# Kernel optimization log

Hardware: AMD Instinct MI355X
Metric: run time of the kernel (lower is better)

The kernel has to match this reference:

```python
import jax, jax.numpy as jnp
import numpy as np
import math

VOCAB, D, H, NL, L, B = 50257, 768, 12, 4, 1024, 2
DH = D // H
DFF = 4 * D
ALPHA = 0.25
NEG = -1e9


def _ln(x, g, b, eps=1e-5):
    mu = x.mean(-1, keepdims=True)
    var = ((x - mu) ** 2).mean(-1, keepdims=True)
    return (x - mu) * jax.lax.rsqrt(var + eps) * g + b


def setup_inputs() -> dict:
    key = jax.random.key(0)
    ks = jax.random.split(key, 16)
    s = 0.02
    tokens = jax.random.randint(ks[0], (B, L), 0, VOCAB)
    timelike_mask = jax.random.randint(ks[1], (NL, D), 0, 2).astype(jnp.int32)
    embed = jax.random.normal(ks[2], (VOCAB, D), jnp.float32) * s
    pos_emb = jax.random.normal(ks[3], (L, D), jnp.float32) * s
    wq = jax.random.normal(ks[4], (NL, D, D), jnp.float32) * s
    wk = jax.random.normal(ks[5], (NL, D, D), jnp.float32) * s
    wv = jax.random.normal(ks[6], (NL, D, D), jnp.float32) * s
    wo = jax.random.normal(ks[7], (NL, D, D), jnp.float32) * s
    ff_w1 = jax.random.normal(ks[8], (NL, DFF, D), jnp.float32) * s
    ff_b1 = jnp.zeros((NL, DFF), jnp.float32)
    ff_w2 = jax.random.normal(ks[9], (NL, D, DFF), jnp.float32) * s
    ff_b2 = jnp.zeros((NL, D), jnp.float32)
    ln1_g = jnp.ones((NL, D), jnp.float32); ln1_b = jnp.zeros((NL, D), jnp.float32)
    ln2_g = jnp.ones((NL, D), jnp.float32); ln2_b = jnp.zeros((NL, D), jnp.float32)
    lnf_g = jnp.ones((D,), jnp.float32); lnf_b = jnp.zeros((D,), jnp.float32)
    return dict(tokens=tokens, timelike_mask=timelike_mask, embed=embed, pos_emb=pos_emb,
                wq=wq, wk=wk, wv=wv, wo=wo,
                ln1_g=ln1_g, ln1_b=ln1_b, ln2_g=ln2_g, ln2_b=ln2_b,
                ff_w1=ff_w1, ff_b1=ff_b1, ff_w2=ff_w2, ff_b2=ff_b2,
                lnf_g=lnf_g, lnf_b=lnf_b)


def reference(tokens, timelike_mask, embed, pos_emb, wq, wk, wv, wo,
              ln1_g, ln1_b, ln2_g, ln2_b, ff_w1, ff_b1, ff_w2, ff_b2,
              lnf_g, lnf_b):
    Bc, Lc = tokens.shape
    scale = math.sqrt(DH)
    # embeddings: token + learned position
    h = embed[tokens] + pos_emb[None, :Lc]  # (B,L,D)
    # additive causal mask, matching torch's -inf attention_mask convention
    causal = jnp.where(jnp.tril(jnp.ones((Lc, Lc), bool)), 0.0, NEG)[None, None]  # (1,1,L,L)
    for i in range(NL):
        xn = _ln(h, ln1_g[i], ln1_b[i])
        # nn.Linear(bias=False): y = x @ W.T, W is (out,in)
        q = jnp.einsum('bld,od->blo', xn, wq[i]).reshape(Bc, Lc, H, DH).astype(jnp.float32)
        k = jnp.einsum('bld,od->blo', xn, wk[i]).reshape(Bc, Lc, H, DH).astype(jnp.float32)
        v = jnp.einsum('bld,od->blo', xn, wv[i]).reshape(Bc, Lc, H, DH)
        # Minkowski term: scores_std - 2*alpha*(Q*P_t)K^T  ==  (Q*(1-2*alpha*m)) K^T
        m = timelike_mask[i].astype(jnp.float32).reshape(H, DH)  # per-head timelike directions
        q_eff = q * (1.0 - 2.0 * ALPHA * m)[None, None]
        scores = jnp.einsum('bqhd,bkhd->bhqk', q_eff, k) / scale + causal
        aw = jax.nn.softmax(scores, axis=-1)  # dropout=0 (eval)
        attn = jnp.einsum('bhqk,bkhd->bqhd', aw, v).reshape(Bc, Lc, D)
        h = h + jnp.einsum('bld,od->blo', attn, wo[i])
        xn2 = _ln(h, ln2_g[i], ln2_b[i])
        ff = jax.nn.gelu(jnp.einsum('bld,fd->blf', xn2, ff_w1[i]) + ff_b1[i], approximate=False)
        h = h + jnp.einsum('blf,df->bld', ff, ff_w2[i]) + ff_b2[i]
    h = _ln(h, lnf_g, lnf_b)
    logits = jnp.einsum('bld,vd->blv', h, embed)  # tied LM head
    return logits
```

## Files before the change

### kernel.cpp

```cpp
#include <hip/hip_runtime.h>
#include <math.h>

#define VOCABSZ 50257
#define VPAD 50432
#define DMODEL 768
#define NHEAD 12
#define NLAYER 4
#define SEQ 1024
#define BATCH 2
#define DHEAD 64
#define DFFN 3072
#define BT (BATCH * SEQ)
#define NBH (BATCH * NHEAD)

typedef __attribute__((ext_vector_type(8))) short bf16x8;
typedef __attribute__((ext_vector_type(4))) float f32x4;

__device__ __forceinline__ ushort f2bf(float f) {
  uint u = __builtin_bit_cast(uint, f);
  u = (u + 0x7fffu + ((u >> 16) & 1u)) >> 16;
  return (ushort)u;
}

__device__ __forceinline__ float bf2f(ushort u) {
  uint x = ((uint)u) << 16;
  return __builtin_bit_cast(float, x);
}

__device__ __forceinline__ void gl_lds16(const ushort* g, ushort* l) {
  __builtin_amdgcn_global_load_lds(
      (const __attribute__((address_space(1))) void*)g,
      (__attribute__((address_space(3))) void*)l, 16, 0, 0);
}

__global__ __launch_bounds__(256) void conv4_kernel(
    const float* __restrict__ src, ushort* __restrict__ dst, int n4) {
  int i = blockIdx.x * 256 + threadIdx.x;
  if (i >= n4) return;
  float4 v = reinterpret_cast<const float4*>(src)[i];
  reinterpret_cast<ushort4*>(dst)[i] =
      make_ushort4(f2bf(v.x), f2bf(v.y), f2bf(v.z), f2bf(v.w));
}

__global__ __launch_bounds__(256) void conv_qkv_kernel(
    const float* __restrict__ src, ushort* __restrict__ dst, int qoff4) {
  const int per4 = DMODEL * DMODEL / 4;
  int i = blockIdx.x * 256 + threadIdx.x;
  if (i >= NLAYER * per4) return;
  int layer = i / per4, rem = i % per4;
  float4 v = reinterpret_cast<const float4*>(src)[i];
  reinterpret_cast<ushort4*>(dst)[(size_t)layer * (3 * per4) + qoff4 + rem] =
      make_ushort4(f2bf(v.x), f2bf(v.y), f2bf(v.z), f2bf(v.w));
}

__global__ __launch_bounds__(256) void conv_embed_kernel(
    const float* __restrict__ emb, ushort* __restrict__ dst) {
  int i = blockIdx.x * 256 + threadIdx.x;
  if (i >= VPAD * DMODEL / 4) return;
  int row = (i * 4) / DMODEL;
  ushort4 o = make_ushort4(0, 0, 0, 0);
  if (row < VOCABSZ) {
    float4 v = reinterpret_cast<const float4*>(emb)[i];
    o = make_ushort4(f2bf(v.x), f2bf(v.y), f2bf(v.z), f2bf(v.w));
  }
  reinterpret_cast<ushort4*>(dst)[i] = o;
}

template <int KS, bool RBIAS, bool EMB>
__global__ __launch_bounds__(256) void ln_kernel(
    float* __restrict__ h, const ushort* __restrict__ part,
    const float* __restrict__ rb, const int* __restrict__ tok,
    const float* __restrict__ emb, const float* __restrict__ pos,
    const float* __restrict__ g, const float* __restrict__ bta,
    ushort* __restrict__ o) {
  __shared__ float red[8];
  int row = blockIdx.x;
  int tid = threadIdx.x;
  float* xr = h + (size_t)row * DMODEL;
  const float* er = nullptr;
  const float* pr = nullptr;
  if (EMB) {
    er = emb + (size_t)tok[row] * DMODEL;
    pr = pos + (size_t)(row & (SEQ - 1)) * DMODEL;
  }
  float v[3];
  float s = 0.f, sq = 0.f;
#pragma unroll
  for (int j = 0; j < 3; ++j) {
    int c = tid + j * 256;
    float a;
    if (EMB) {
      a = er[c] + pr[c];
      xr[c] = a;
    } else {
      a = xr[c];
      if (RBIAS) a += rb[c];
      if (KS > 0) {
#pragma unroll
        for (int z = 0; z < KS; ++z)
          a += bf2f(part[(size_t)z * BT * DMODEL + (size_t)row * DMODEL + c]);
        xr[c] = a;
      }
    }
    v[j] = a;
    s += a;
    sq += a * a;
  }
#pragma unroll
  for (int off = 1; off < 64; off <<= 1) {
    s += __shfl_xor(s, off);
    sq += __shfl_xor(sq, off);
  }
  int wid = tid >> 6;
  if ((tid & 63) == 0) { red[wid * 2] = s; red[wid * 2 + 1] = sq; }
  __syncthreads();
  float S = red[0] + red[2] + red[4] + red[6];
  float SQ = red[1] + red[3] + red[5] + red[7];
  float mu = S * (1.0f / DMODEL);
  float var = SQ * (1.0f / DMODEL) - mu * mu;
  float r = rsqrtf(var + 1e-5f);
  ushort* orow = o + (size_t)row * DMODEL;
#pragma unroll
  for (int j = 0; j < 3; ++j) {
    int c = tid + j * 256;
    orow[c] = f2bf((v[j] - mu) * r * g[c] + bta[c]);
  }
}

__global__ __launch_bounds__(256) void fattn_kernel(
    const ushort* __restrict__ q, const ushort* __restrict__ k,
    const ushort* __restrict__ vt, ushort* __restrict__ o) {
  __shared__ __align__(16) ushort Ks[2][64 * 64];
  __shared__ __align__(16) ushort Vs[2][64 * 64];
  __shared__ __align__(16) ushort Ps[4][16][80];
  const int bid = blockIdx.x;
  const int wgid = (bid & 7) * 48 + (bid >> 3);
  const int z = wgid / 16, qb_ = wgid % 16;
  const int b = z / NHEAD, hh = z % NHEAD;
  const int q0 = (15 - qb_) * 64;
  const int tid = threadIdx.x, w = tid >> 6, l = tid & 63;
  const int fr = l & 15, ks = l >> 4;
  const int qrow = q0 + w * 16 + fr;
  const ushort* qp = q + (size_t)(b * SEQ + qrow) * DMODEL + hh * DHEAD;
  const bf16x8 qf0 = *reinterpret_cast<const bf16x8*>(qp + ks * 8);
  const bf16x8 qf1 = *reinterpret_cast<const bf16x8*>(qp + 32 + ks * 8);

  const int srow = w * 16 + (l >> 3);
  const int g0 = ((l & 7) ^ (srow & 7)) * 8;

  auto stage = [&](int k0, int d) {
#pragma unroll
    for (int c = 0; c < 2; ++c) {
      int r = srow + c * 8;
      gl_lds16(k + (size_t)(b * SEQ + k0 + r) * DMODEL + hh * DHEAD + g0,
               &Ks[d][(w * 16 + c * 8) * 64]);
      gl_lds16(vt + (size_t)(z * 64 + r) * SEQ + k0 + g0,
               &Vs[d][(w * 16 + c * 8) * 64]);
    }
  };

  f32x4 acc_o[4] = {};
  float mrun = -1e30f, lrun = 0.f;
  const int nt = q0 >> 6;

  stage(0, 0);
  for (int t = 0; t <= nt; ++t) {
    const int cur = t & 1;
    if (t < nt) {
      stage((t + 1) * 64, cur ^ 1);
      asm volatile("s_waitcnt vmcnt(4)" ::: "memory");
    } else {
      asm volatile("s_waitcnt vmcnt(0)" ::: "memory");
    }
    __builtin_amdgcn_s_barrier();
    __builtin_amdgcn_sched_barrier(0);
    f32x4 acc_s[4] = {};
#pragma unroll
    for (int kstep = 0; kstep < 2; ++kstep) {
      const bf16x8 qf = kstep ? qf1 : qf0;
#pragma unroll
      for (int kb = 0; kb < 4; ++kb) {
        int ra = kb * 16 + fr;
        bf16x8 af = *reinterpret_cast<const bf16x8*>(
            &Ks[cur][ra * 64 + (((kstep * 4 + ks) ^ (ra & 7)) * 8)]);
        acc_s[kb] =
            __builtin_amdgcn_mfma_f32_16x16x32_bf16(af, qf, acc_s[kb], 0, 0, 0);
      }
    }
    const bool diag = (t == nt);
    float pm = -1e30f;
    float sv[4][4];
#pragma unroll
    for (int kb = 0; kb < 4; ++kb)
#pragma unroll
      for (int r = 0; r < 4; ++r) {
        float s = acc_s[kb][r];
        if (diag && (q0 + kb * 16 + ks * 4 + r > qrow)) s = -1e30f;
        sv[kb][r] = s;
        pm = fmaxf(pm, s);
      }
    pm = fmaxf(pm, __shfl_xor(pm, 16));
    pm = fmaxf(pm, __shfl_xor(pm, 32));
    if (!__all(pm - mrun <= 8.0f)) {
      float mnew = fmaxf(mrun, pm);
      float scale = __expf(mrun - mnew);
      lrun *= scale;
#pragma unroll
      for (int db = 0; db < 4; ++db) acc_o[db] *= scale;
      mrun = mnew;
    }
    float psum = 0.f;
#pragma unroll
    for (int kb = 0; kb < 4; ++kb) {
      float p0 = __expf(sv[kb][0] - mrun);
      float p1 = __expf(sv[kb][1] - mrun);
      float p2 = __expf(sv[kb][2] - mrun);
      float p3 = __expf(sv[kb][3] - mrun);
      psum += (p0 + p1) + (p2 + p3);
      *reinterpret_cast<ushort4*>(&Ps[w][fr][kb * 16 + ks * 4]) =
          make_ushort4(f2bf(p0), f2bf(p1), f2bf(p2), f2bf(p3));
    }
    psum += __shfl_xor(psum, 16);
    psum += __shfl_xor(psum, 32);
    lrun += psum;
#pragma unroll
    for (int kstep = 0; kstep < 2; ++kstep) {
      bf16x8 pf =
          *reinterpret_cast<const bf16x8*>(&Ps[w][fr][kstep * 32 + ks * 8]);
#pragma unroll
      for (int db = 0; db < 4; ++db) {
        int rd = db * 16 + fr;
        bf16x8 vf = *reinterpret_cast<const bf16x8*>(
            &Vs[cur][rd * 64 + (((kstep * 4 + ks) ^ (rd & 7)) * 8)]);
        acc_o[db] =
            __builtin_amdgcn_mfma_f32_16x16x32_bf16(vf, pf, acc_o[db], 0, 0, 0);
      }
    }
    __builtin_amdgcn_sched_barrier(0);
    __builtin_amdgcn_s_barrier();
  }
  float rinv = 1.0f / lrun;
#pragma unroll
  for (int db = 0; db < 4; ++db) {
    ushort4 o4 =
        make_ushort4(f2bf(acc_o[db][0] * rinv), f2bf(acc_o[db][1] * rinv),
                     f2bf(acc_o[db][2] * rinv), f2bf(acc_o[db][3] * rinv));
    *reinterpret_cast<ushort4*>(o + (size_t)(b * SEQ + qrow) * DMODEL +
                                hh * DHEAD + db * 16 + ks * 4) = o4;
  }
}

template <bool QKV, bool BIAS, bool GELU, bool RES, bool OUTBF, bool SWZ,
          bool PART>
__global__ __launch_bounds__(256) void gemm_bf16_nt(
    const ushort* __restrict__ A, const ushort* __restrict__ B,
    const float* __restrict__ bias, const int* __restrict__ tmask,
    const float* __restrict__ res, float* __restrict__ Cf,
    ushort* __restrict__ Cb, int ldc, ushort* __restrict__ qb,
    ushort* __restrict__ kb, ushort* __restrict__ vt, int M, int K, int Nreal,
    int kchunk) {
  __shared__ __align__(16) ushort As[2][128 * 32];
  __shared__ __align__(16) ushort Bs[2][128 * 32];
  int bnx, bmy;
  if (SWZ) {
    int bid = blockIdx.x;
    int chunk = gridDim.x >> 3;
    int wgid = (bid & 7) * chunk + (bid >> 3);
    int mb = M >> 7;
    bmy = wgid % mb;
    bnx = wgid / mb;
  } else {
    bnx = blockIdx.x;
    bmy = blockIdx.y;
  }
  const int m0 = bmy * 128, n0 = bnx * 128;
  const int kbeg = PART ? blockIdx.z * kchunk : 0;
  const int kend = PART ? kbeg + kchunk : K;
  if (PART) Cb += (size_t)blockIdx.z * M * ldc;
  const int tid = threadIdx.x;
  const int w = tid >> 6, l = tid & 63;
  const int wr = w >> 1, wc = w & 1;
  const int fr = l & 15, ks = l >> 4;

  const int seg0 = w * 2, seg1 = w * 2 + 1;
  const int srow0 = seg0 * 16 + (l >> 2);
  const int srow1 = seg1 * 16 + (l >> 2);
  const int koff0 = (((l & 3) ^ ((srow0 >> 1) & 3))) * 8;
  const int koff1 = (((l & 3) ^ ((srow1 >> 1) & 3))) * 8;
  const ushort* A0 = A + (size_t)(m0 + srow0) * K + koff0;
  const ushort* A1 = A + (size_t)(m0 + srow1) * K + koff1;
  const ushort* B0 = B + (size_t)(n0 + srow0) * K + koff0;
  const ushort* B1 = B + (size_t)(n0 + srow1) * K + koff1;

  int aoff[4], boff[4];
#pragma unroll
  for (int i = 0; i < 4; ++i) {
    int ra = wr * 64 + i * 16 + fr;
    aoff[i] = ra * 32 + ((ks ^ ((ra >> 1) & 3)) * 8);
    int rb = wc * 64 + i * 16 + fr;
    boff[i] = rb * 32 + ((ks ^ ((rb >> 1) & 3)) * 8);
  }

  gl_lds16(A0 + kbeg, &As[0][seg0 * 512]);
  gl_lds16(A1 + kbeg, &As[0][seg1 * 512]);
  gl_lds16(B0 + kbeg, &Bs[0][seg0 * 512]);
  gl_lds16(B1 + kbeg, &Bs[0][seg1 * 512]);

  f32x4 acc[4][4] = {};
  int cur = 0;
  for (int k0 = kbeg; k0 < kend; k0 += 32) {
    const int nxt = k0 + 32;
    if (nxt < kend) {
      gl_lds16(A0 + nxt, &As[cur ^ 1][seg0 * 512]);
      gl_lds16(A1 + nxt, &As[cur ^ 1][seg1 * 512]);
      gl_lds16(B0 + nxt, &Bs[cur ^ 1][seg0 * 512]);
      gl_lds16(B1 + nxt, &Bs[cur ^ 1][seg1 * 512]);
      asm volatile("s_waitcnt vmcnt(4)" ::: "memory");
    } else {
      asm volatile("s_waitcnt vmcnt(0)" ::: "memory");
    }
    __builtin_amdgcn_s_barrier();
    __builtin_amdgcn_sched_barrier(0);
    bf16x8 af[4], bfr[4];
#pragma unroll
    for (int i = 0; i < 4; ++i)
      af[i] = *reinterpret_cast<const bf16x8*>(&As[cur][aoff[i]]);
#pragma unroll
    for (int i = 0; i < 4; ++i)
      bfr[i] = *reinterpret_cast<const bf16x8*>(&Bs[cur][boff[i]]);
#pragma unroll
    for (int mi = 0; mi < 4; ++mi)
#pragma unroll
      for (int nj = 0; nj < 4; ++nj)
        acc[mi][nj] = __builtin_amdgcn_mfma_f32_16x16x32_bf16(
            af[mi], bfr[nj], acc[mi][nj], 0, 0, 0);
    __builtin_amdgcn_sched_barrier(0);
    __builtin_amdgcn_s_barrier();
    cur ^= 1;
  }

#pragma unroll
  for (int mi = 0; mi < 4; ++mi) {
#pragma unroll
    for (int nj = 0; nj < 4; ++nj) {
      int n = n0 + wc * 64 + nj * 16 + fr;
      if (n < Nreal) {
        if (PART) {
#pragma unroll
          for (int r = 0; r < 4; ++r) {
            int m = m0 + wr * 64 + mi * 16 + ks * 4 + r;
            Cb[(size_t)m * ldc + n] = f2bf(acc[mi][nj][r]);
          }
        } else if (QKV) {
          if (n < DMODEL) {
            float sc = (1.0f - 0.5f * (float)tmask[n]) * 0.125f;
#pragma unroll
            for (int r = 0; r < 4; ++r) {
              int m = m0 + wr * 64 + mi * 16 + ks * 4 + r;
              qb[(size_t)m * DMODEL + n] = f2bf(acc[mi][nj][r] * sc);
            }
          } else if (n < 2 * DMODEL) {
#pragma unroll
            for (int r = 0; r < 4; ++r) {
              int m = m0 + wr * 64 + mi * 16 + ks * 4 + r;
              kb[(size_t)m * DMODEL + (n - DMODEL)] = f2bf(acc[mi][nj][r]);
            }
          } else {
            int d = n - 2 * DMODEL;
            int key = (m0 & (SEQ - 1)) + wr * 64 + mi * 16 + ks * 4;
            size_t zr = (size_t)((m0 >> 10) * NHEAD + (d >> 6)) * 64 + (d & 63);
            ushort4 p4 = make_ushort4(
                f2bf(acc[mi][nj][0]), f2bf(acc[mi][nj][1]),
                f2bf(acc[mi][nj][2]), f2bf(acc[mi][nj][3]));
            *reinterpret_cast<ushort4*>(vt + zr * SEQ + key) = p4;
          }
        } else {
#pragma unroll
          for (int r = 0; r < 4; ++r) {
            int m = m0 + wr * 64 + mi * 16 + ks * 4 + r;
            float v = acc[mi][nj][r];
            if (BIAS) v += bias[n];
            if (GELU) v = 0.5f * v * (1.0f + erff(v * 0.70710678118f));
            if (RES) v += res[(size_t)m * ldc + n];
            if (OUTBF)
              Cb[(size_t)m * ldc + n] = f2bf(v);
            else
              Cf[(size_t)m * ldc + n] = v;
          }
        }
      }
    }
  }
}

__global__ __launch_bounds__(512, 2) void gemm_lmhead(
    const ushort* __restrict__ A, const ushort* __restrict__ B,
    float* __restrict__ C) {
  __shared__ __align__(16) ushort SMEM[4 * 256 * 64];
  const int K = DMODEL;
  const int NTILE = K / 64;
  const int ITERS = NTILE / 2;

  const int bid = blockIdx.x;
  const int chunk = gridDim.x >> 3;
  const int wgid = (bid & 7) * chunk + (bid >> 3);
  const int m0 = (wgid & 7) * 256;
  const int n0 = (wgid >> 3) * 256;

  const int tid = threadIdx.x;
  const int w = tid >> 6, l = tid & 63;
  const int wr = w >> 2, wc = w & 3;
  const int fr = l & 15, ks = l >> 4;

  const int strow = tid >> 3;
  const int stk = ((tid & 7) ^ (strow & 7)) * 8;
  const int wseg = (w << 3) * 64;

  const int fsw0 = (ks ^ (fr & 7)) * 8;
  const int fsw1 = ((4 | ks) ^ (fr & 7)) * 8;
  const int arow = (wr * 128 + fr) * 64;
  const int brow = (wc * 64 + fr) * 64;

  bf16x8 Ar[4][2], Br[4][2];
  f32x4 acc[8][4] = {};

#define STA(d, kt, rb)                                            \
  gl_lds16(A + (size_t)(m0 + (rb) + strow) * K + (kt) * 64 + stk, \
           SMEM + (d) * 16384 + (rb) * 64 + wseg)
#define STB(d, kt, rb)                                            \
  gl_lds16(B + (size_t)(n0 + (rb) + strow) * K + (kt) * 64 + stk, \
           SMEM + 32768 + (d) * 16384 + (rb) * 64 + wseg)
#define RDA(d, mi, kst)                           \
  (*reinterpret_cast<const bf16x8*>(              \
      &SMEM[(d) * 16384 + arow + (mi) * 1024 + ((kst) ? fsw1 : fsw0)]))
#define RDB(d, nj, kst)                           \
  (*reinterpret_cast<const bf16x8*>(              \
      &SMEM[32768 + (d) * 16384 + brow + (nj) * 1024 + ((kst) ? fsw1 : fsw0)]))
#define MMAQ(mh, nh)                                                       \
  _Pragma("unroll") for (int kst = 0; kst < 2; ++kst)                      \
  _Pragma("unroll") for (int mi = 0; mi < 4; ++mi)                         \
  _Pragma("unroll") for (int nj = 0; nj < 2; ++nj)                         \
    acc[(mh)*4 + mi][(nh)*2 + nj] = __builtin_amdgcn_mfma_f32_16x16x32_bf16( \
        Ar[mi][kst], Br[(nh)*2 + nj][kst], acc[(mh)*4 + mi][(nh)*2 + nj],  \
        0, 0, 0)
#define BAR __builtin_amdgcn_s_barrier()
#define PRIO1 __builtin_amdgcn_s_setprio(1)
#define PRIO0 __builtin_amdgcn_s_setprio(0)

  STA(0, 0, 0); STA(0, 0, 64); STA(0, 0, 128); STA(0, 0, 192);
  STB(0, 0, 0); STB(0, 0, 64); STB(0, 0, 128); STB(0, 0, 192);
  STB(1, 1, 0); STB(1, 1, 64); STB(1, 1, 128); STB(1, 1, 192);
  asm volatile("s_waitcnt vmcnt(4)" ::: "memory");
  BAR;

  for (int it = 0; it < ITERS; ++it) {
    const int t1 = 2 * it + 1;
    const int tn = 2 * it + 2;
    const bool s0 = tn < NTILE, s1 = tn + 1 < NTILE;
#pragma unroll
    for (int mi = 0; mi < 4; ++mi) {
      Ar[mi][0] = RDA(0, mi, 0); Ar[mi][1] = RDA(0, mi, 1);
    }
#pragma unroll
    for (int nj = 0; nj < 2; ++nj) {
      Br[nj][0] = RDB(0, nj, 0); Br[nj][1] = RDB(0, nj, 1);
    }
    STA(1, t1, 0); STA(1, t1, 64);
    BAR; PRIO1; MMAQ(0, 0); PRIO0; BAR;
#pragma unroll
    for (int nj = 2; nj < 4; ++nj) {
      Br[nj][0] = RDB(0, nj, 0); Br[nj][1] = RDB(0, nj, 1);
    }
    STA(1, t1, 128); STA(1, t1, 192);
    BAR; PRIO1; MMAQ(0, 1); PRIO0; BAR;
#pragma unroll
    for (int mi = 0; mi < 4; ++mi) {
      Ar[mi][0] = RDA(0, mi + 4, 0); Ar[mi][1] = RDA(0, mi + 4, 1);
    }
    if (s0) { STB(0, tn, 0); STB(0, tn, 64); }
    BAR; PRIO1; MMAQ(1, 1); PRIO0; BAR;
    if (s0) { STB(0, tn, 128); STB(0, tn, 192); }
    BAR; PRIO1; MMAQ(1, 0); PRIO0;
    if (s0)
      asm volatile("s_waitcnt vmcnt(4)" ::: "memory");
    else
      asm volatile("s_waitcnt vmcnt(0)" ::: "memory");
    BAR;
#pragma unroll
    for (int mi = 0; mi < 4; ++mi) {
      Ar[mi][0] = RDA(1, mi, 0); Ar[mi][1] = RDA(1, mi, 1);
    }
#pragma unroll
    for (int nj = 0; nj < 2; ++nj) {
      Br[nj][0] = RDB(1, nj, 0); Br[nj][1] = RDB(1, nj, 1);
    }
    if (s0) { STA(0, tn, 0); STA(0, tn, 64); }
    BAR; PRIO1; MMAQ(0, 0); PRIO0; BAR;
#pragma unroll
    for (int nj = 2; nj < 4; ++nj) {
      Br[nj][0] = RDB(1, nj, 0); Br[nj][1] = RDB(1, nj, 1);
    }
    if (s0) { STA(0, tn, 128); STA(0, tn, 192); }
    BAR; PRIO1; MMAQ(0, 1); PRIO0; BAR;
#pragma unroll
    for (int mi = 0; mi < 4; ++mi) {
      Ar[mi][0] = RDA(1, mi + 4, 0); Ar[mi][1] = RDA(1, mi + 4, 1);
    }
    if (s1) { STB(1, tn + 1, 0); STB(1, tn + 1, 64); }
    BAR; PRIO1; MMAQ(1, 1); PRIO0; BAR;
    if (s1) { STB(1, tn + 1, 128); STB(1, tn + 1, 192); }
    BAR; PRIO1; MMAQ(1, 0); PRIO0;
    if (it + 1 < ITERS) {
      asm volatile("s_waitcnt vmcnt(4)" ::: "memory");
      BAR;
    }
  }

  float* eb = reinterpret_cast<float*>(SMEM);
#pragma unroll 1
  for (int p = 0; p < 2; ++p) {
    __syncthreads();
    if (wr == p) {
#pragma unroll
      for (int mi = 0; mi < 8; ++mi)
#pragma unroll
        for (int nj = 0; nj < 4; ++nj)
#pragma unroll
          for (int r = 0; r < 4; ++r)
            eb[(mi * 16 + ks * 4 + r) * 256 + wc * 64 + nj * 16 + fr] =
                acc[mi][nj][r];
    }
    __syncthreads();
    const size_t rowbase = (size_t)(m0 + p * 128) * VOCABSZ + n0;
#pragma unroll 8
    for (int c = 0; c < 64; ++c) {
      int lin = c * 512 + tid;
      int row = lin >> 8, col = lin & 255;
      if (n0 + col < VOCABSZ) {
        __builtin_nontemporal_store(
            eb[lin], C + rowbase + (size_t)row * VOCABSZ + col);
      }
    }
  }
#undef STA
#undef STB
#undef RDA
#undef RDB
#undef MMAQ
#undef BAR
#undef PRIO1
#undef PRIO0
}

extern "C" void kernel_launch(void* const* d_in, const int* in_sizes, int n_in,
                              void* d_out, int out_size, void* d_ws,
                              size_t ws_size, hipStream_t stream) {
  const int* tokens = (const int*)d_in[0];
  const int* tmask = (const int*)d_in[1];
  const float* embed = (const float*)d_in[2];
  const float* pos = (const float*)d_in[3];
  const float* wq = (const float*)d_in[4];
  const float* wk = (const float*)d_in[5];
  const float* wv = (const float*)d_in[6];
  const float* wo = (const float*)d_in[7];
  const float* ln1g = (const float*)d_in[8];
  const float* ln1b = (const float*)d_in[9];
  const float* ln2g = (const float*)d_in[10];
  const float* ln2b = (const float*)d_in[11];
  const float* fw1 = (const float*)d_in[12];
  const float* fb1 = (const float*)d_in[13];
  const float* fw2 = (const float*)d_in[14];
  const float* fb2 = (const float*)d_in[15];
  const float* lnfg = (const float*)d_in[16];
  const float* lnfb = (const float*)d_in[17];

  char* wp = (char*)d_ws;
  auto alloc = [&](size_t bytes) {
    void* p = wp;
    wp += (bytes + 255) & ~(size_t)255;
    return p;
  };
  float* h = (float*)alloc((size_t)BT * DMODEL * 4);
  ushort* part = (ushort*)alloc((size_t)4 * BT * DMODEL * 2);
  ushort* qb = (ushort*)alloc((size_t)BT * DMODEL * 2);
  ushort* kb = (ushort*)alloc((size_t)BT * DMODEL * 2);
  ushort* vt = (ushort*)alloc((size_t)NBH * DHEAD * SEQ * 2);
  ushort* xn = (ushort*)alloc((size_t)BT * DMODEL * 2);
  ushort* ab = (ushort*)alloc((size_t)BT * DMODEL * 2);
  ushort* ffb = (ushort*)alloc((size_t)BT * DFFN * 2);
  ushort* wqkv_b = (ushort*)alloc((size_t)NLAYER * 3 * DMODEL * DMODEL * 2);
  ushort* wo_b = (ushort*)alloc((size_t)NLAYER * DMODEL * DMODEL * 2);
  ushort* fw1_b = (ushort*)alloc((size_t)NLAYER * DFFN * DMODEL * 2);
  ushort* fw2_b = (ushort*)alloc((size_t)NLAYER * DMODEL * DFFN * 2);
  ushort* emb_b = (ushort*)alloc((size_t)VPAD * DMODEL * 2);

  const int per4 = DMODEL * DMODEL / 4;
  conv_qkv_kernel<<<(NLAYER * per4 + 255) / 256, 256, 0, stream>>>(wq, wqkv_b, 0);
  conv_qkv_kernel<<<(NLAYER * per4 + 255) / 256, 256, 0, stream>>>(wk, wqkv_b, per4);
  conv_qkv_kernel<<<(NLAYER * per4 + 255) / 256, 256, 0, stream>>>(wv, wqkv_b, 2 * per4);
  conv4_kernel<<<(NLAYER * per4 + 255) / 256, 256, 0, stream>>>(wo, wo_b, NLAYER * per4);
  const int nff4 = NLAYER * DFFN * DMODEL / 4;
  conv4_kernel<<<(nff4 + 255) / 256, 256, 0, stream>>>(fw1, fw1_b, nff4);
  conv4_kernel<<<(nff4 + 255) / 256, 256, 0, stream>>>(fw2, fw2_b, nff4);
  conv_embed_kernel<<<(VPAD * DMODEL / 4 + 255) / 256, 256, 0, stream>>>(embed, emb_b);

  const dim3 gqkv(3 * DMODEL / 128, BT / 128);
  const dim3 gff(DFFN / 128, BT / 128);
  const dim3 gwo(DMODEL / 128, BT / 128, 2);
  const dim3 gff2(DMODEL / 128, BT / 128, 4);

  for (int i = 0; i < NLAYER; ++i) {
    if (i == 0)
      ln_kernel<0, false, true><<<BT, 256, 0, stream>>>(
          h, nullptr, nullptr, tokens, embed, pos, ln1g, ln1b, xn);
    else
      ln_kernel<4, true, false><<<BT, 256, 0, stream>>>(
          h, part, fb2 + (i - 1) * DMODEL, nullptr, nullptr, nullptr,
          ln1g + i * DMODEL, ln1b + i * DMODEL, xn);

    gemm_bf16_nt<true, false, false, false, false, false, false>
        <<<gqkv, 256, 0, stream>>>(
            xn, wqkv_b + (size_t)i * 3 * DMODEL * DMODEL, nullptr,
            tmask + i * DMODEL, nullptr, nullptr, nullptr, 0, qb, kb, vt, BT,
            DMODEL, 3 * DMODEL, DMODEL);

    fattn_kernel<<<NBH * (SEQ / 64), 256, 0, stream>>>(qb, kb, vt, ab);

    gemm_bf16_nt<false, false, false, false, false, false, true>
        <<<gwo, 256, 0, stream>>>(
            ab, wo_b + (size_t)i * DMODEL * DMODEL, nullptr, nullptr, nullptr,
            nullptr, part, DMODEL, nullptr, nullptr, nullptr, BT, DMODEL,
            DMODEL, DMODEL / 2);

    ln_kernel<2, false, false><<<BT, 256, 0, stream>>>(
        h, part, nullptr, nullptr, nullptr, nullptr, ln2g + i * DMODEL,
        ln2b + i * DMODEL, xn);

    gemm_bf16_nt<false, true, true, false, true, false, false>
        <<<gff, 256, 0, stream>>>(
            xn, fw1_b + (size_t)i * DFFN * DMODEL, fb1 + i * DFFN, nullptr,
            nullptr, nullptr, ffb, DFFN, nullptr, nullptr, nullptr, BT, DMODEL,
            DFFN, DMODEL);

    gemm_bf16_nt<false, false, false, false, false, false, true>
        <<<gff2, 256, 0, stream>>>(
            ffb, fw2_b + (size_t)i * DMODEL * DFFN, nullptr, nullptr, nullptr,
            nullptr, part, DMODEL, nullptr, nullptr, nullptr, BT, DFFN, DMODEL,
            DFFN / 4);
  }

  ln_kernel<4, true, false><<<BT, 256, 0, stream>>>(
      h, part, fb2 + (NLAYER - 1) * DMODEL, nullptr, nullptr, nullptr, lnfg,
      lnfb, xn);

  gemm_lmhead<<<8 * (VPAD / 256), 512, 0, stream>>>(xn, emb_b, (float*)d_out);
}
```

Baseline: 855.6 us.

## Merge weight conversion launches and halve FF2 split-K partials

Replaces the six per-tensor weight conversion launches with two combined kernels, one for Q/K/V and one for Wo/W1/W2, to cut launch overhead. It also lowers the split-K factor of the second FFN GEMM from 4 to 2, which shrinks the partial buffer and the reduction work in the following layernorm kernels. The trade-off is fewer workgroups and longer K loops in the FF2 GEMM, which may hurt occupancy on a GPU with many compute units.

```diff
diff --git a/kernel.cpp b/kernel.cpp
--- a/kernel.cpp
+++ b/kernel.cpp
@@ -33,23 +33,44 @@
       (__attribute__((address_space(3))) void*)l, 16, 0, 0);
 }
 
-__global__ __launch_bounds__(256) void conv4_kernel(
-    const float* __restrict__ src, ushort* __restrict__ dst, int n4) {
+__global__ __launch_bounds__(256) void conv_qkv3_kernel(
+    const float* __restrict__ wq, const float* __restrict__ wk,
+    const float* __restrict__ wv, ushort* __restrict__ dst) {
+  const int per4 = DMODEL * DMODEL / 4;
+  const int total = NLAYER * per4;
   int i = blockIdx.x * 256 + threadIdx.x;
-  if (i >= n4) return;
-  float4 v = reinterpret_cast<const float4*>(src)[i];
-  reinterpret_cast<ushort4*>(dst)[i] =
+  if (i >= 3 * total) return;
+  int which = i / total;
+  int rem = i - which * total;
+  const float* src = (which == 0) ? wq : (which == 1) ? wk : wv;
+  int layer = rem / per4, r2 = rem % per4;
+  float4 v = reinterpret_cast<const float4*>(src)[rem];
+  reinterpret_cast<ushort4*>(dst)[(size_t)layer * (3 * per4) + which * per4 +
+                                  r2] =
       make_ushort4(f2bf(v.x), f2bf(v.y), f2bf(v.z), f2bf(v.w));
 }
 
-__global__ __launch_bounds__(256) void conv_qkv_kernel(
-    const float* __restrict__ src, ushort* __restrict__ dst, int qoff4) {
-  const int per4 = DMODEL * DMODEL / 4;
+__global__ __launch_bounds__(256) void conv3_kernel(
+    const float* __restrict__ wo, ushort* __restrict__ wo_b,
+    const float* __restrict__ fw1, ushort* __restrict__ fw1_b,
+    const float* __restrict__ fw2, ushort* __restrict__ fw2_b) {
+  const int n1 = NLAYER * DMODEL * DMODEL / 4;
+  const int nf = NLAYER * DFFN * DMODEL / 4;
   int i = blockIdx.x * 256 + threadIdx.x;
-  if (i >= NLAYER * per4) return;
-  int layer = i / per4, rem = i % per4;
-  float4 v = reinterpret_cast<const float4*>(src)[i];
-  reinterpret_cast<ushort4*>(dst)[(size_t)layer * (3 * per4) + qoff4 + rem] =
+  const float* src;
+  ushort* dst;
+  int idx;
+  if (i < n1) {
+    src = wo; dst = wo_b; idx = i;
+  } else if (i < n1 + nf) {
+    src = fw1; dst = fw1_b; idx = i - n1;
+  } else if (i < n1 + 2 * nf) {
+    src = fw2; dst = fw2_b; idx = i - n1 - nf;
+  } else {
+    return;
+  }
+  float4 v = reinterpret_cast<const float4*>(src)[idx];
+  reinterpret_cast<ushort4*>(dst)[idx] =
       make_ushort4(f2bf(v.x), f2bf(v.y), f2bf(v.z), f2bf(v.w));
 }
 
@@ -581,7 +602,7 @@
     return p;
   };
   float* h = (float*)alloc((size_t)BT * DMODEL * 4);
-  ushort* part = (ushort*)alloc((size_t)4 * BT * DMODEL * 2);
+  ushort* part = (ushort*)alloc((size_t)2 * BT * DMODEL * 2);
   ushort* qb = (ushort*)alloc((size_t)BT * DMODEL * 2);
   ushort* kb = (ushort*)alloc((size_t)BT * DMODEL * 2);
   ushort* vt = (ushort*)alloc((size_t)NBH * DHEAD * SEQ * 2);
@@ -595,26 +616,25 @@
   ushort* emb_b = (ushort*)alloc((size_t)VPAD * DMODEL * 2);
 
   const int per4 = DMODEL * DMODEL / 4;
-  conv_qkv_kernel<<<(NLAYER * per4 + 255) / 256, 256, 0, stream>>>(wq, wqkv_b, 0);
-  conv_qkv_kernel<<<(NLAYER * per4 + 255) / 256, 256, 0, stream>>>(wk, wqkv_b, per4);
-  conv_qkv_kernel<<<(NLAYER * per4 + 255) / 256, 256, 0, stream>>>(wv, wqkv_b, 2 * per4);
-  conv4_kernel<<<(NLAYER * per4 + 255) / 256, 256, 0, stream>>>(wo, wo_b, NLAYER * per4);
   const int nff4 = NLAYER * DFFN * DMODEL / 4;
-  conv4_kernel<<<(nff4 + 255) / 256, 256, 0, stream>>>(fw1, fw1_b, nff4);
-  conv4_kernel<<<(nff4 + 255) / 256, 256, 0, stream>>>(fw2, fw2_b, nff4);
-  conv_embed_kernel<<<(VPAD * DMODEL / 4 + 255) / 256, 256, 0, stream>>>(embed, emb_b);
+  conv_qkv3_kernel<<<(3 * NLAYER * per4 + 255) / 256, 256, 0, stream>>>(
+      wq, wk, wv, wqkv_b);
+  conv3_kernel<<<(NLAYER * per4 + 2 * nff4 + 255) / 256, 256, 0, stream>>>(
+      wo, wo_b, fw1, fw1_b, fw2, fw2_b);
+  conv_embed_kernel<<<(VPAD * DMODEL / 4 + 255) / 256, 256, 0, stream>>>(
+      embed, emb_b);
 
   const dim3 gqkv(3 * DMODEL / 128, BT / 128);
   const dim3 gff(DFFN / 128, BT / 128);
   const dim3 gwo(DMODEL / 128, BT / 128, 2);
-  const dim3 gff2(DMODEL / 128, BT / 128, 4);
+  const dim3 gff2(DMODEL / 128, BT / 128, 2);
 
   for (int i = 0; i < NLAYER; ++i) {
     if (i == 0)
       ln_kernel<0, false, true><<<BT, 256, 0, stream>>>(
           h, nullptr, nullptr, tokens, embed, pos, ln1g, ln1b, xn);
     else
-      ln_kernel<4, true, false><<<BT, 256, 0, stream>>>(
+      ln_kernel<2, true, false><<<BT, 256, 0, stream>>>(
           h, part, fb2 + (i - 1) * DMODEL, nullptr, nullptr, nullptr,
           ln1g + i * DMODEL, ln1b + i * DMODEL, xn);
 
@@ -646,10 +666,10 @@
         <<<gff2, 256, 0, stream>>>(
             ffb, fw2_b + (size_t)i * DMODEL * DFFN, nullptr, nullptr, nullptr,
             nullptr, part, DMODEL, nullptr, nullptr, nullptr, BT, DFFN, DMODEL,
-            DFFN / 4);
-  }
-
-  ln_kernel<4, true, false><<<BT, 256, 0, stream>>>(
+            DFFN / 2);
+  }
+
+  ln_kernel<2, true, false><<<BT, 256, 0, stream>>>(
       h, part, fb2 + (NLAYER - 1) * DMODEL, nullptr, nullptr, nullptr, lnfg,
       lnfb, xn);
 
```

Result: slower. 895.0 us (+4.6%).
